# Kernel tuning notes

Hardware: AMD Instinct MI355X
Metric: run time of the kernel (lower is better)

Reference implementation:

```python
import jax, jax.numpy as jnp
import numpy as np

B, N, C = 2, 2048, 1024
H, HD = 16, 64
PX, PY, PS = 24, 24, 16  # S2RoPE head_dim split (px+py+ps == head_dim)


def rotate_half(t):
    t1, t2 = jnp.split(t, 2, axis=-1)
    return jnp.concatenate([-t2, t1], axis=-1)


def apply_phase_rope(t, phase):
    # t: [B, N, H, d_seg] (d_seg even), phase: [B, N, d_seg//2] angles in radians
    ang = jnp.concatenate([phase, phase], axis=-1)[:, :, None, :]  # [B,N,1,d_seg]
    return t * jnp.cos(ang) + rotate_half(t) * jnp.sin(ang)


def s2rope(t, phase_x, phase_y, phase_sph):
    # spherical RoPE: rotate three disjoint segments of head_dim by the
    # per-token x / y / spherical phases
    tx, ty, ts = t[..., :PX], t[..., PX:PX + PY], t[..., PX + PY:]
    return jnp.concatenate([
        apply_phase_rope(tx, phase_x),
        apply_phase_rope(ty, phase_y),
        apply_phase_rope(ts, phase_sph),
    ], axis=-1)


def setup_inputs() -> dict:
    key = jax.random.key(0)
    ks = jax.random.split(key, 9)
    two_pi = 6.2831853
    return {
        "x": jax.random.normal(ks[0], (B, N, C), dtype=jnp.float32),
        "phase_x": jax.random.uniform(ks[1], (B, N, PX // 2), dtype=jnp.float32) * two_pi,
        "phase_y": jax.random.uniform(ks[2], (B, N, PY // 2), dtype=jnp.float32) * two_pi,
        "phase_sph": jax.random.uniform(ks[3], (B, N, PS // 2), dtype=jnp.float32) * two_pi,
        "rope_mask": jax.random.randint(ks[4], (B, N), 0, 2).astype(bool),
        "Wqkv": jax.random.normal(ks[5], (C, 3 * C), dtype=jnp.float32) * (C ** -0.5),
        "bqkv": jax.random.normal(ks[6], (3 * C,), dtype=jnp.float32) * 0.02,
        "Wproj": jax.random.normal(ks[7], (C, C), dtype=jnp.float32) * (C ** -0.5),
        "bproj": jax.random.normal(ks[8], (C,), dtype=jnp.float32) * 0.02,
    }


def reference(x, phase_x, phase_y, phase_sph, rope_mask, Wqkv, bqkv, Wproj, bproj):
    # qkv projection -> [B, N, 3, H, HD]
    qkv = (x @ Wqkv + bqkv).reshape(B, N, 3, H, HD)
    q, k, v = qkv[:, :, 0], qkv[:, :, 1], qkv[:, :, 2]  # each [B, N, H, HD]

    # template path: S2RoPE with rope_mask selecting which tokens are rotated
    q_rope = s2rope(q, phase_x, phase_y, phase_sph)
    k_rope = s2rope(k, phase_x, phase_y, phase_sph)
    m = rope_mask[:, :, None, None]  # [B, N, 1, 1]
    q = jnp.where(m, q_rope, q)
    k = jnp.where(m, k_rope, k)

    scale = HD ** -0.5
    # [B, H, N, N] scores, softmax over keys, then weighted sum of values
    attn = jax.nn.softmax(jnp.einsum('bnhd,bmhd->bhnm', q, k) * scale, axis=-1)
    out = jnp.einsum('bhnm,bmhd->bnhd', attn, v).reshape(B, N, C)
    return out @ Wproj + bproj
```

## Files before the change

### kernel.cpp

```cpp
#include <hip/hip_runtime.h>
#include <hip/hip_fp16.h>

typedef _Float16 f16;
typedef unsigned int u32;
typedef _Float16 f16x4 __attribute__((ext_vector_type(4)));
typedef _Float16 f16x8 __attribute__((ext_vector_type(8)));
typedef float f32x4 __attribute__((ext_vector_type(4)));
typedef float f32x16 __attribute__((ext_vector_type(16)));

#define B_  2
#define N_  2048
#define C_  1024
#define H_  16
#define HD_ 64

__device__ __forceinline__ void gload_lds16(const void* g, void* l) {
  __builtin_amdgcn_global_load_lds((const __attribute__((address_space(1))) u32*)g,
                                   (__attribute__((address_space(3))) u32*)l,
                                   16, 0, 0);
}

__device__ __forceinline__ u32 pack_f16(float a, float b) {
  auto h2 = __builtin_amdgcn_cvt_pkrtz(a, b);
  return __builtin_bit_cast(u32, h2);
}

__device__ __forceinline__ float max3f(float a, float b, float c) {
  return fmaxf(fmaxf(a, b), c);
}

__global__ void detect_mask(const u32* __restrict__ m, int* __restrict__ flag) {
  __shared__ int bad;
  if (threadIdx.x == 0) bad = 0;
  __syncthreads();
  int v = 0;
  for (int i = threadIdx.x; i < 1024; i += 256) {
    u32 w = m[i];
    if (w != 0u && w != 1u && w != 0x3F800000u) v = 1;
  }
  if (v) atomicOr(&bad, 1);
  __syncthreads();
  if (threadIdx.x == 0) *flag = bad;
}

__global__ __launch_bounds__(256) void phase_tab(const float* __restrict__ px,
                                                 const float* __restrict__ py,
                                                 const float* __restrict__ psp,
                                                 const void* __restrict__ maskPtr,
                                                 const int* __restrict__ maskFlag,
                                                 float* __restrict__ cs_tab,
                                                 float* __restrict__ sn_tab) {
  const int idx = blockIdx.x * 256 + threadIdx.x;
  const int j = idx & 31, tn = idx >> 5;
  const int byteMode = *maskFlag;
  const bool doRope = byteMode ? (((const unsigned char*)maskPtr)[tn] != 0)
                               : (((const u32*)maskPtr)[tn] != 0u);
  float c = 1.f, s = 0.f;
  if (doRope) {
    float ph;
    if (j < 12)      ph = px[tn * 12 + j];
    else if (j < 24) ph = py[tn * 12 + (j - 12)];
    else             ph = psp[tn * 8 + (j - 24)];
    c = __cosf(ph);
    s = __sinf(ph);
  }
  cs_tab[idx] = c;
  sn_tab[idx] = s;
}

__global__ __launch_bounds__(256) void cvt_x(const float* __restrict__ in,
                                             f16* __restrict__ out, int n8) {
  const int i = blockIdx.x * 256 + threadIdx.x;
  if (i >= n8) return;
  const float4 a = ((const float4*)in)[i * 2];
  const float4 b = ((const float4*)in)[i * 2 + 1];
  f16x8 o = {(f16)a.x, (f16)a.y, (f16)a.z, (f16)a.w,
             (f16)b.x, (f16)b.y, (f16)b.z, (f16)b.w};
  ((f16x8*)out)[i] = o;
}

__global__ __launch_bounds__(256) void transpose_cvt(const float* __restrict__ W,
                                                     f16* __restrict__ Wt,
                                                     int R, int Ccols) {
  __shared__ __align__(16) f16 tile[32][34];
  const int c0 = blockIdx.x * 32, r0 = blockIdx.y * 32;
  const int tx = threadIdx.x, ty = threadIdx.y;
#pragma unroll
  for (int k = 0; k < 4; ++k)
    tile[ty + 8 * k][tx] = (f16)W[(size_t)(r0 + ty + 8 * k) * Ccols + c0 + tx];
  __syncthreads();
#pragma unroll
  for (int k = 0; k < 4; ++k)
    Wt[(size_t)(c0 + ty + 8 * k) * R + r0 + tx] = tile[tx][ty + 8 * k];
}

__global__ __launch_bounds__(256) void gemm_qkv(const f16* __restrict__ A,
                                                const f16* __restrict__ Bt,
                                                const float* __restrict__ bias,
                                                const float* __restrict__ cs_tab,
                                                const float* __restrict__ sn_tab,
                                                f16* __restrict__ Qh,
                                                f16* __restrict__ Kh,
                                                f16* __restrict__ Vt) {
  __shared__ __align__(16) f16 smem[128 * 130];
  f16* const As = smem;
  f16* const Bs = smem + 8192;
  const int K = 1024, Ncols = 3072;
  const int tid = threadIdx.x;
  const int lane = tid & 63;
  const int wv = tid >> 6;
  const int wm = wv >> 1, wn = wv & 1;
  const int nTN = Ncols >> 7;
  int bid = blockIdx.x;
  const int cpx = gridDim.x >> 3;
  bid = (bid & 7) * cpx + (bid >> 3);
  const int tM = bid / nTN, tN = bid % nTN;
  const int rowBase = tM << 7, colBase = tN << 7;
  const int cl = lane & 15, cg = lane >> 4;

  f32x4 acc[4][4];
#pragma unroll
  for (int i = 0; i < 4; ++i)
#pragma unroll
    for (int j = 0; j < 4; ++j) acc[i][j] = (f32x4){0.f, 0.f, 0.f, 0.f};

  const int sR = tid >> 3, sC = tid & 7;

  for (int k0 = 0; k0 < K; k0 += 64) {
#pragma unroll
    for (int is = 0; is < 4; ++is) {
      const int r = is * 32 + sR;
      const int sc = sC ^ (r & 7);
      gload_lds16(A + (size_t)(rowBase + r) * K + k0 + sc * 8, As + is * 2048 + tid * 8);
    }
#pragma unroll
    for (int is = 0; is < 4; ++is) {
      const int r = is * 32 + sR;
      const int sc = sC ^ (r & 7);
      gload_lds16(Bt + (size_t)(colBase + r) * K + k0 + sc * 8, Bs + is * 2048 + tid * 8);
    }
    asm volatile("s_waitcnt vmcnt(0)" ::: "memory");
    __syncthreads();

#pragma unroll
    for (int ks = 0; ks < 2; ++ks) {
      f16x8 af[4], bf[4];
#pragma unroll
      for (int m = 0; m < 4; ++m) {
        const int row = wm * 64 + m * 16 + cl;
        const int ck = (ks * 4 + cg) ^ (row & 7);
        af[m] = *(const f16x8*)(As + row * 64 + ck * 8);
      }
#pragma unroll
      for (int n = 0; n < 4; ++n) {
        const int row = wn * 64 + n * 16 + cl;
        const int ck = (ks * 4 + cg) ^ (row & 7);
        bf[n] = *(const f16x8*)(Bs + row * 64 + ck * 8);
      }
#pragma unroll
      for (int m = 0; m < 4; ++m)
#pragma unroll
        for (int n = 0; n < 4; ++n)
          acc[m][n] = __builtin_amdgcn_mfma_f32_16x16x32_f16(af[m], bf[n], acc[m][n], 0, 0, 0);
    }
    __syncthreads();
  }

#pragma unroll
  for (int m = 0; m < 4; ++m)
#pragma unroll
    for (int n = 0; n < 4; ++n) {
      const int lc = wn * 64 + n * 16 + cl;
      const float bz = bias[colBase + lc];
#pragma unroll
      for (int reg = 0; reg < 4; ++reg) {
        const int lr = wm * 64 + m * 16 + cg * 4 + reg;
        smem[lr * 130 + lc] = (f16)(acc[m][n][reg] + bz);
      }
    }
  __syncthreads();

  const int sec = colBase >> 10;
  const int h0 = (colBase & 1023) >> 6;
  const int bb = rowBase >> 11;
  const int nbase = rowBase & 2047;

  if (sec < 2) {
    const int lr = tid >> 1, hh = tid & 1;
    const int n = nbase + lr;
    const int h = h0 + hh;
    const f16* srcrow = smem + lr * 130 + hh * 64;
    float t[64];
#pragma unroll
    for (int c = 0; c < 8; ++c) {
      f16x8 v = *(const f16x8*)(srcrow + c * 8);
#pragma unroll
      for (int j = 0; j < 8; ++j) t[c * 8 + j] = (float)v[j];
    }
    const float* csr = cs_tab + ((size_t)bb * N_ + n) * 32;
    const float* snr = sn_tab + ((size_t)bb * N_ + n) * 32;
    __align__(16) f16 o[64];
#pragma unroll
    for (int d = 0; d < 64; ++d) {
      int j;
      float rot;
      if (d < 24) {
        j = (d < 12) ? d : d - 12;
        rot = (d < 12) ? -t[d + 12] : t[d - 12];
      } else if (d < 48) {
        const int dd = d - 24;
        j = 12 + ((dd < 12) ? dd : dd - 12);
        rot = (dd < 12) ? -t[d + 12] : t[d - 12];
      } else {
        const int dd = d - 48;
        j = 24 + ((dd < 8) ? dd : dd - 8);
        rot = (dd < 8) ? -t[d + 8] : t[d - 8];
      }
      o[d] = (f16)(t[d] * csr[j] + rot * snr[j]);
    }
    f16* dst = (sec == 0 ? Qh : Kh) + (((size_t)(bb * H_ + h)) * N_ + n) * 64;
#pragma unroll
    for (int c = 0; c < 8; ++c) *(f16x8*)(dst + c * 8) = *(const f16x8*)(o + c * 8);
  } else {
    const int pr = tid >> 1, half = tid & 1;
    const int hh = pr >> 6, d = pr & 63;
    const int h = h0 + hh;
    __align__(16) f16 o[64];
#pragma unroll
    for (int i = 0; i < 64; ++i) o[i] = smem[(half * 64 + i) * 130 + hh * 64 + d];
    f16* dst = Vt + (((size_t)(bb * H_ + h)) * 64 + d) * N_ + nbase + half * 64;
#pragma unroll
    for (int c = 0; c < 8; ++c) *(f16x8*)(dst + c * 8) = *(const f16x8*)(o + c * 8);
  }
}

__global__ __launch_bounds__(256) void gemm_bt_f32(const f16* __restrict__ A,
                                                   const f16* __restrict__ Bt,
                                                   const float* __restrict__ bias,
                                                   float* __restrict__ Cout,
                                                   int M, int N, int K) {
  __shared__ __align__(16) f16 As[128 * 64];
  __shared__ __align__(16) f16 Bs[128 * 64];
  const int tid = threadIdx.x;
  const int lane = tid & 63;
  const int wv = tid >> 6;
  const int wm = wv >> 1, wn = wv & 1;
  const int nTN = N >> 7;
  int bid = blockIdx.x;
  const int cpx = gridDim.x >> 3;
  bid = (bid & 7) * cpx + (bid >> 3);
  const int tM = bid / nTN, tN = bid % nTN;
  const int rowBase = tM << 7, colBase = tN << 7;
  const int cl = lane & 15, cg = lane >> 4;

  f32x4 acc[4][4];
#pragma unroll
  for (int i = 0; i < 4; ++i)
#pragma unroll
    for (int j = 0; j < 4; ++j) acc[i][j] = (f32x4){0.f, 0.f, 0.f, 0.f};

  const int sR = tid >> 3, sC = tid & 7;

  for (int k0 = 0; k0 < K; k0 += 64) {
#pragma unroll
    for (int is = 0; is < 4; ++is) {
      const int r = is * 32 + sR;
      const int sc = sC ^ (r & 7);
      gload_lds16(A + (size_t)(rowBase + r) * K + k0 + sc * 8, As + is * 2048 + tid * 8);
    }
#pragma unroll
    for (int is = 0; is < 4; ++is) {
      const int r = is * 32 + sR;
      const int sc = sC ^ (r & 7);
      gload_lds16(Bt + (size_t)(colBase + r) * K + k0 + sc * 8, Bs + is * 2048 + tid * 8);
    }
    asm volatile("s_waitcnt vmcnt(0)" ::: "memory");
    __syncthreads();

#pragma unroll
    for (int ks = 0; ks < 2; ++ks) {
      f16x8 af[4], bf[4];
#pragma unroll
      for (int m = 0; m < 4; ++m) {
        const int row = wm * 64 + m * 16 + cl;
        const int ck = (ks * 4 + cg) ^ (row & 7);
        af[m] = *(const f16x8*)(As + row * 64 + ck * 8);
      }
#pragma unroll
      for (int n = 0; n < 4; ++n) {
        const int row = wn * 64 + n * 16 + cl;
        const int ck = (ks * 4 + cg) ^ (row & 7);
        bf[n] = *(const f16x8*)(Bs + row * 64 + ck * 8);
      }
#pragma unroll
      for (int m = 0; m < 4; ++m)
#pragma unroll
        for (int n = 0; n < 4; ++n)
          acc[m][n] = __builtin_amdgcn_mfma_f32_16x16x32_f16(af[m], bf[n], acc[m][n], 0, 0, 0);
    }
    __syncthreads();
  }

#pragma unroll
  for (int m = 0; m < 4; ++m) {
#pragma unroll
    for (int n = 0; n < 4; ++n) {
      const int gr0 = rowBase + wm * 64 + m * 16 + cg * 4;
      const int gc = colBase + wn * 64 + n * 16 + cl;
      const float bz = bias[gc];
#pragma unroll
      for (int reg = 0; reg < 4; ++reg)
        Cout[(size_t)(gr0 + reg) * N + gc] = acc[m][n][reg] + bz;
    }
  }
}

__global__ __launch_bounds__(256) void attn2(const f16* __restrict__ Qh,
                                             const f16* __restrict__ Kh,
                                             const f16* __restrict__ Vt,
                                             f16* __restrict__ Y) {
  __shared__ __align__(16) f16 lds_flat[3 * 8192];
  const int tid = threadIdx.x, lane = tid & 63, w = tid >> 6;
  int bid = blockIdx.x;
  bid = (bid & 7) * 64 + (bid >> 3);
  const int bh = bid >> 4, qb = bid & 15;
  const int b = bh >> 4, h = bh & 15;
  const f16* Qb = Qh + (size_t)bh * N_ * 64;
  const f16* Kb = Kh + (size_t)bh * N_ * 64;
  const f16* Vb = Vt + (size_t)bh * 64 * N_;
  const int ql = lane & 31, hi = lane >> 5;

  f16x8 qf[4];
  {
    const int qrow = qb * 128 + w * 32 + ql;
    const f16 scl = (f16)0.125f;
#pragma unroll
    for (int ks = 0; ks < 4; ++ks) {
      f16x8 v = *(const f16x8*)(Qb + (size_t)qrow * 64 + ks * 16 + hi * 8);
#pragma unroll
      for (int j = 0; j < 8; ++j) v[j] *= scl;
      qf[ks] = v;
    }
  }

  f32x16 Of[2];
#pragma unroll
  for (int d = 0; d < 2; ++d)
#pragma unroll
    for (int r = 0; r < 16; ++r) Of[d][r] = 0.f;
  float m_run = -1e30f, l_run = 0.f;

  const int sr = tid >> 3, sc = tid & 7;
#define STAGE(t, bp)                                                                     \
  {                                                                                      \
    _Pragma("unroll") for (int i = 0; i < 2; ++i) {                                      \
      const int row = i * 32 + sr;                                                       \
      const int g = sc ^ (row & 7);                                                      \
      gload_lds16(Kb + (size_t)((t) * 64 + row) * 64 + g * 8, (bp) + i * 2048 + tid * 8);\
    }                                                                                    \
    _Pragma("unroll") for (int i = 0; i < 2; ++i) {                                      \
      const int row = i * 32 + sr;                                                       \
      const int g = sc ^ (row & 7);                                                      \
      gload_lds16(Vb + (size_t)row * N_ + (t) * 64 + g * 8,                              \
                  (bp) + 4096 + i * 2048 + tid * 8);                                     \
    }                                                                                    \
  }

#define SOFTMAX_CHUNK(sa)                                                                \
  {                                                                                      \
    float t0 = max3f(sa[0], sa[1], sa[2]);                                               \
    float t1 = max3f(sa[3], sa[4], sa[5]);                                               \
    float t2 = max3f(sa[6], sa[7], sa[8]);                                               \
    float t3 = max3f(sa[9], sa[10], sa[11]);                                             \
    float t4 = max3f(sa[12], sa[13], sa[14]);                                            \
    float pmax = max3f(max3f(t0, t1, t2), max3f(t3, t4, sa[15]), -1e30f);                \
    pmax = fmaxf(pmax, __shfl_xor(pmax, 32));                                            \
    if (__any(pmax > m_run + 8.0f)) {                                                    \
      const float mnew = fmaxf(m_run, pmax);                                             \
      const float corr = __expf(m_run - mnew);                                           \
      l_run *= corr;                                                                     \
      _Pragma("unroll") for (int d = 0; d < 2; ++d)                                      \
        _Pragma("unroll") for (int r = 0; r < 16; ++r) Of[d][r] *= corr;                 \
      m_run = mnew;                                                                      \
    }                                                                                    \
    _Pragma("unroll") for (int r = 0; r < 16; ++r) sa[r] = __expf(sa[r] - m_run);        \
    float s0 = ((sa[0] + sa[1]) + (sa[2] + sa[3])) + ((sa[4] + sa[5]) + (sa[6] + sa[7]));\
    float s1 = ((sa[8] + sa[9]) + (sa[10] + sa[11])) +                                   \
               ((sa[12] + sa[13]) + (sa[14] + sa[15]));                                  \
    l_run += s0 + s1;                                                                    \
  }

#define PV_CHUNK(sa, s)                                                                  \
  {                                                                                      \
    u32 pw[8];                                                                           \
    _Pragma("unroll") for (int tt = 0; tt < 8; ++tt)                                     \
      pw[tt] = pack_f16(sa[2 * tt], sa[2 * tt + 1]);                                     \
    _Pragma("unroll") for (int kk = 0; kk < 2; ++kk) {                                   \
      u32 a0 = pw[4 * kk], a1 = pw[4 * kk + 1];                                          \
      u32 b0 = pw[4 * kk + 2], b1 = pw[4 * kk + 3];                                      \
      asm volatile("v_permlane32_swap_b32 %0, %1" : "+v"(a0), "+v"(b0));                 \
      asm volatile("v_permlane32_swap_b32 %0, %1" : "+v"(a1), "+v"(b1));                 \
      union { u32 u[4]; f16x8 v; } pf;                                                   \
      pf.u[0] = a0; pf.u[1] = a1; pf.u[2] = b0; pf.u[3] = b1;                            \
      __builtin_amdgcn_s_setprio(1);                                                     \
      _Pragma("unroll") for (int df = 0; df < 2; ++df) {                                 \
        const int d = df * 32 + ql;                                                      \
        f16x8 vf = *(const f16x8*)(Vs + d * 64 + (((s) * 4 + kk * 2 + hi) ^ (d & 7)) * 8);\
        Of[df] = __builtin_amdgcn_mfma_f32_32x32x16_f16(vf, pf.v, Of[df], 0, 0, 0);      \
      }                                                                                  \
      __builtin_amdgcn_s_setprio(0);                                                     \
    }                                                                                    \
  }

  f16* const base = &lds_flat[0];
  STAGE(0, base);
  STAGE(1, base + 8192);
  asm volatile("s_waitcnt vmcnt(4)" ::: "memory");
  __builtin_amdgcn_s_barrier();

  f16* curp = base;
  f16* stagep = base + 16384;
  for (int t = 0; t < N_ / 64; ++t) {
    if (t < N_ / 64 - 2) STAGE(t + 2, stagep);
    const f16* Ks = curp;
    const f16* Vs = curp + 4096;

    f32x16 sa0, sa1;
#pragma unroll
    for (int r = 0; r < 16; ++r) { sa0[r] = 0.f; sa1[r] = 0.f; }
    const int krow0 = ql, krow1 = 32 + ql;
    __builtin_amdgcn_s_setprio(1);
#pragma unroll
    for (int ks = 0; ks < 4; ++ks) {
      f16x8 kf = *(const f16x8*)(Ks + krow0 * 64 + ((ks * 2 + hi) ^ (krow0 & 7)) * 8);
      sa0 = __builtin_amdgcn_mfma_f32_32x32x16_f16(kf, qf[ks], sa0, 0, 0, 0);
    }
#pragma unroll
    for (int ks = 0; ks < 4; ++ks) {
      f16x8 kf = *(const f16x8*)(Ks + krow1 * 64 + ((ks * 2 + hi) ^ (krow1 & 7)) * 8);
      sa1 = __builtin_amdgcn_mfma_f32_32x32x16_f16(kf, qf[ks], sa1, 0, 0, 0);
    }
    __builtin_amdgcn_s_setprio(0);

    SOFTMAX_CHUNK(sa0);
    PV_CHUNK(sa0, 0);
    SOFTMAX_CHUNK(sa1);
    PV_CHUNK(sa1, 1);

    if (t < N_ / 64 - 2)
      asm volatile("s_waitcnt vmcnt(4) lgkmcnt(0)" ::: "memory");
    else if (t < N_ / 64 - 1)
      asm volatile("s_waitcnt vmcnt(0) lgkmcnt(0)" ::: "memory");
    else
      asm volatile("s_waitcnt lgkmcnt(0)" ::: "memory");
    __builtin_amdgcn_s_barrier();
    curp = (curp == base + 16384) ? base : curp + 8192;
    stagep = (stagep == base + 16384) ? base : stagep + 8192;
  }

  const float l_tot = l_run + __shfl_xor(l_run, 32);
  const float inv = 1.0f / l_tot;
  f16* Ow = base + w * (32 * 72);
#pragma unroll
  for (int df = 0; df < 2; ++df)
#pragma unroll
    for (int g = 0; g < 4; ++g) {
      f16x4 ov;
#pragma unroll
      for (int e = 0; e < 4; ++e) ov[e] = (f16)(Of[df][g * 4 + e] * inv);
      *(f16x4*)(Ow + ql * 72 + df * 32 + g * 8 + hi * 4) = ov;
    }
  __syncthreads();
  const int rr = lane >> 1, half = lane & 1;
  const f16* srcp = Ow + rr * 72 + half * 32;
  const int nglob = qb * 128 + w * 32 + rr;
  f16* dst = Y + ((size_t)b * N_ + nglob) * C_ + h * 64 + half * 32;
#pragma unroll
  for (int c2 = 0; c2 < 4; ++c2)
    *(f16x8*)(dst + c2 * 8) = *(const f16x8*)(srcp + c2 * 8);
}

extern "C" void kernel_launch(void* const* d_in, const int* in_sizes, int n_in,
                              void* d_out, int out_size, void* d_ws, size_t ws_size,
                              hipStream_t stream) {
  const float* x = (const float*)d_in[0];
  const float* px = (const float*)d_in[1];
  const float* py = (const float*)d_in[2];
  const float* psp = (const float*)d_in[3];
  const void* mask = (const void*)d_in[4];
  const float* Wqkv = (const float*)d_in[5];
  const float* bqkv = (const float*)d_in[6];
  const float* Wproj = (const float*)d_in[7];
  const float* bproj = (const float*)d_in[8];
  float* out = (float*)d_out;
  char* ws = (char*)d_ws;

  f16* xh     = (f16*)(ws + 0);
  f16* Wqkvt  = (f16*)(ws + 8388608);
  f16* Wprojt = (f16*)(ws + 14680064);
  f16* Qh     = (f16*)(ws + 41943040);
  f16* Kh     = (f16*)(ws + 50331648);
  f16* Vt     = (f16*)(ws + 58720256);
  f16* Yh     = (f16*)(ws + 67108864);
  int* mflag  = (int*)(ws + 75497472);
  float* cs_tab = (float*)(ws + 16777216);
  float* sn_tab = (float*)(ws + 16777216 + 524288);

  detect_mask<<<1, 256, 0, stream>>>((const u32*)mask, mflag);
  cvt_x<<<2048, 256, 0, stream>>>(x, xh, (B_ * N_ * C_) / 8);
  phase_tab<<<512, 256, 0, stream>>>(px, py, psp, mask, mflag, cs_tab, sn_tab);
  transpose_cvt<<<dim3(96, 32), dim3(32, 8), 0, stream>>>(Wqkv, Wqkvt, C_, 3 * C_);
  transpose_cvt<<<dim3(32, 32), dim3(32, 8), 0, stream>>>(Wproj, Wprojt, C_, C_);
  gemm_qkv<<<(4096 / 128) * (3072 / 128), 256, 0, stream>>>(
      xh, Wqkvt, bqkv, cs_tab, sn_tab, Qh, Kh, Vt);
  attn2<<<512, 256, 0, stream>>>(Qh, Kh, Vt, Yh);
  gemm_bt_f32<<<(4096 / 128) * (1024 / 128), 256, 0, stream>>>(
      Yh, Wprojt, bproj, out, 4096, 1024, 1024);
}
```

Measured before the change: 153.1 us.

## Split attention over two KV halves and merge partials in a combine kernel

Splits each attention block's key/value range into two halves (flash-decoding style). This doubles the grid to 1024 blocks, so the 256 CUs of MI355X get more than two waves' worth of blocks and the tail is better balanced. Each half writes a normalized partial output plus its (max, sum) to workspace, and a new combine kernel rescales and merges the two into Y. The cost is extra global traffic for partials and statistics, one more kernel launch, and repeated Q loads.

```diff
diff --git a/kernel.cpp b/kernel.cpp
--- a/kernel.cpp
+++ b/kernel.cpp
@@ -315,19 +315,23 @@
   }
 }
 
+#define NT_ 16
 __global__ __launch_bounds__(256) void attn2(const f16* __restrict__ Qh,
                                              const f16* __restrict__ Kh,
                                              const f16* __restrict__ Vt,
-                                             f16* __restrict__ Y) {
+                                             f16* __restrict__ Op,
+                                             float2* __restrict__ Ml) {
   __shared__ __align__(16) f16 lds_flat[3 * 8192];
   const int tid = threadIdx.x, lane = tid & 63, w = tid >> 6;
   int bid = blockIdx.x;
-  bid = (bid & 7) * 64 + (bid >> 3);
-  const int bh = bid >> 4, qb = bid & 15;
+  bid = (bid & 7) * 128 + (bid >> 3);
+  const int bh = bid >> 5;
+  const int qb = (bid >> 1) & 15;
+  const int kvh = bid & 1;
   const int b = bh >> 4, h = bh & 15;
   const f16* Qb = Qh + (size_t)bh * N_ * 64;
-  const f16* Kb = Kh + (size_t)bh * N_ * 64;
-  const f16* Vb = Vt + (size_t)bh * 64 * N_;
+  const f16* Kb = Kh + (size_t)bh * N_ * 64 + (size_t)kvh * 1024 * 64;
+  const f16* Vb = Vt + (size_t)bh * 64 * N_ + (size_t)kvh * 1024;
   const int ql = lane & 31, hi = lane >> 5;
 
   f16x8 qf[4];
@@ -420,8 +424,8 @@
 
   f16* curp = base;
   f16* stagep = base + 16384;
-  for (int t = 0; t < N_ / 64; ++t) {
-    if (t < N_ / 64 - 2) STAGE(t + 2, stagep);
+  for (int t = 0; t < NT_; ++t) {
+    if (t < NT_ - 2) STAGE(t + 2, stagep);
     const f16* Ks = curp;
     const f16* Vs = curp + 4096;
 
@@ -447,9 +451,9 @@
     SOFTMAX_CHUNK(sa1);
     PV_CHUNK(sa1, 1);
 
-    if (t < N_ / 64 - 2)
+    if (t < NT_ - 2)
       asm volatile("s_waitcnt vmcnt(4) lgkmcnt(0)" ::: "memory");
-    else if (t < N_ / 64 - 1)
+    else if (t < NT_ - 1)
       asm volatile("s_waitcnt vmcnt(0) lgkmcnt(0)" ::: "memory");
     else
       asm volatile("s_waitcnt lgkmcnt(0)" ::: "memory");
@@ -460,6 +464,9 @@
 
   const float l_tot = l_run + __shfl_xor(l_run, 32);
   const float inv = 1.0f / l_tot;
+  const int part = kvh * 32 + bh;
+  if (hi == 0)
+    Ml[(size_t)part * N_ + qb * 128 + w * 32 + ql] = make_float2(m_run, l_tot);
   f16* Ow = base + w * (32 * 72);
 #pragma unroll
   for (int df = 0; df < 2; ++df)
@@ -474,10 +481,38 @@
   const int rr = lane >> 1, half = lane & 1;
   const f16* srcp = Ow + rr * 72 + half * 32;
   const int nglob = qb * 128 + w * 32 + rr;
-  f16* dst = Y + ((size_t)b * N_ + nglob) * C_ + h * 64 + half * 32;
+  f16* dst = Op + ((size_t)part * N_ + nglob) * 64 + half * 32;
 #pragma unroll
   for (int c2 = 0; c2 < 4; ++c2)
     *(f16x8*)(dst + c2 * 8) = *(const f16x8*)(srcp + c2 * 8);
+}
+
+__global__ __launch_bounds__(256) void combine(const f16* __restrict__ Op,
+                                               const float2* __restrict__ Ml,
+                                               f16* __restrict__ Y) {
+  const int gid = blockIdx.x * 256 + threadIdx.x;
+  const int r = gid >> 1, part = gid & 1;
+  const int bh = r >> 11, n = r & 2047;
+  const int b = bh >> 4, h = bh & 15;
+  const float2 ml0 = Ml[(size_t)bh * N_ + n];
+  const float2 ml1 = Ml[(size_t)(32 + bh) * N_ + n];
+  const float m = fmaxf(ml0.x, ml1.x);
+  float w0 = ml0.y * __expf(ml0.x - m);
+  float w1 = ml1.y * __expf(ml1.x - m);
+  const float inv = 1.0f / (w0 + w1);
+  w0 *= inv; w1 *= inv;
+  const f16* o0 = Op + ((size_t)bh * N_ + n) * 64 + part * 32;
+  const f16* o1 = Op + ((size_t)(32 + bh) * N_ + n) * 64 + part * 32;
+  f16* dst = Y + ((size_t)b * N_ + n) * C_ + h * 64 + part * 32;
+#pragma unroll
+  for (int c = 0; c < 4; ++c) {
+    const f16x8 a = ((const f16x8*)o0)[c];
+    const f16x8 bv = ((const f16x8*)o1)[c];
+    f16x8 o;
+#pragma unroll
+    for (int j = 0; j < 8; ++j) o[j] = (f16)((float)a[j] * w0 + (float)bv[j] * w1);
+    ((f16x8*)dst)[c] = o;
+  }
 }
 
 extern "C" void kernel_launch(void* const* d_in, const int* in_sizes, int n_in,
@@ -503,8 +538,10 @@
   f16* Vt     = (f16*)(ws + 58720256);
   f16* Yh     = (f16*)(ws + 67108864);
   int* mflag  = (int*)(ws + 75497472);
-  float* cs_tab = (float*)(ws + 16777216);
-  float* sn_tab = (float*)(ws + 16777216 + 524288);
+  float*  cs_tab = (float*)(ws + 16777216);
+  float*  sn_tab = (float*)(ws + 17301504);
+  f16*    Op     = (f16*)(ws + 17825792);
+  float2* Ml     = (float2*)(ws + 34603008);
 
   detect_mask<<<1, 256, 0, stream>>>((const u32*)mask, mflag);
   cvt_x<<<2048, 256, 0, stream>>>(x, xh, (B_ * N_ * C_) / 8);
@@ -513,7 +550,8 @@
   transpose_cvt<<<dim3(32, 32), dim3(32, 8), 0, stream>>>(Wproj, Wprojt, C_, C_);
   gemm_qkv<<<(4096 / 128) * (3072 / 128), 256, 0, stream>>>(
       xh, Wqkvt, bqkv, cs_tab, sn_tab, Qh, Kh, Vt);
-  attn2<<<512, 256, 0, stream>>>(Qh, Kh, Vt, Yh);
+  attn2<<<1024, 256, 0, stream>>>(Qh, Kh, Vt, Op, Ml);
+  combine<<<512, 256, 0, stream>>>(Op, Ml, Yh);
   gemm_bt_f32<<<(4096 / 128) * (1024 / 128), 256, 0, stream>>>(
       Yh, Wprojt, bproj, out, 4096, 1024, 1024);
 }
```

Result: slower. 160.1 us (+4.6%).

## Load K and V fragments directly from global memory instead of LDS staging

Applied to the files above, without the earlier changes.

The attention kernel drops its triple-buffered async global-to-LDS staging of K and V tiles, along with the per-iteration barriers and waitcnts. Each wave now reads its K and V MFMA fragments straight from global memory, relying on L2 and cache hits since the four waves in a block share the same K/V. This removes synchronisation and LDS traffic but gives up explicit prefetch, so load latency now sits on the critical path. The V reads are strided by row across N, which can make them poorly coalesced.

```diff
diff --git a/kernel.cpp b/kernel.cpp
--- a/kernel.cpp
+++ b/kernel.cpp
@@ -315,11 +315,11 @@
   }
 }
 
-__global__ __launch_bounds__(256) void attn2(const f16* __restrict__ Qh,
+__global__ __launch_bounds__(256) void attn3(const f16* __restrict__ Qh,
                                              const f16* __restrict__ Kh,
                                              const f16* __restrict__ Vt,
                                              f16* __restrict__ Y) {
-  __shared__ __align__(16) f16 lds_flat[3 * 8192];
+  __shared__ __align__(16) f16 Owlds[4][32 * 72];
   const int tid = threadIdx.x, lane = tid & 63, w = tid >> 6;
   int bid = blockIdx.x;
   bid = (bid & 7) * 64 + (bid >> 3);
@@ -349,22 +349,6 @@
 #pragma unroll
     for (int r = 0; r < 16; ++r) Of[d][r] = 0.f;
   float m_run = -1e30f, l_run = 0.f;
-
-  const int sr = tid >> 3, sc = tid & 7;
-#define STAGE(t, bp)                                                                     \
-  {                                                                                      \
-    _Pragma("unroll") for (int i = 0; i < 2; ++i) {                                      \
-      const int row = i * 32 + sr;                                                       \
-      const int g = sc ^ (row & 7);                                                      \
-      gload_lds16(Kb + (size_t)((t) * 64 + row) * 64 + g * 8, (bp) + i * 2048 + tid * 8);\
-    }                                                                                    \
-    _Pragma("unroll") for (int i = 0; i < 2; ++i) {                                      \
-      const int row = i * 32 + sr;                                                       \
-      const int g = sc ^ (row & 7);                                                      \
-      gload_lds16(Vb + (size_t)row * N_ + (t) * 64 + g * 8,                              \
-                  (bp) + 4096 + i * 2048 + tid * 8);                                     \
-    }                                                                                    \
-  }
 
 #define SOFTMAX_CHUNK(sa)                                                                \
   {                                                                                      \
@@ -405,62 +389,45 @@
       __builtin_amdgcn_s_setprio(1);                                                     \
       _Pragma("unroll") for (int df = 0; df < 2; ++df) {                                 \
         const int d = df * 32 + ql;                                                      \
-        f16x8 vf = *(const f16x8*)(Vs + d * 64 + (((s) * 4 + kk * 2 + hi) ^ (d & 7)) * 8);\
+        f16x8 vf = *(const f16x8*)(Vb + (size_t)d * N_ + t * 64 +                        \
+                                   ((s) * 4 + kk * 2 + hi) * 8);                         \
         Of[df] = __builtin_amdgcn_mfma_f32_32x32x16_f16(vf, pf.v, Of[df], 0, 0, 0);      \
       }                                                                                  \
       __builtin_amdgcn_s_setprio(0);                                                     \
     }                                                                                    \
   }
 
-  f16* const base = &lds_flat[0];
-  STAGE(0, base);
-  STAGE(1, base + 8192);
-  asm volatile("s_waitcnt vmcnt(4)" ::: "memory");
-  __builtin_amdgcn_s_barrier();
-
-  f16* curp = base;
-  f16* stagep = base + 16384;
+#pragma unroll 2
   for (int t = 0; t < N_ / 64; ++t) {
-    if (t < N_ / 64 - 2) STAGE(t + 2, stagep);
-    const f16* Ks = curp;
-    const f16* Vs = curp + 4096;
+    const f16* Kr0 = Kb + (size_t)(t * 64 + ql) * 64 + hi * 8;
+    const f16* Kr1 = Kb + (size_t)(t * 64 + 32 + ql) * 64 + hi * 8;
+    f16x8 k0[4], k1[4];
+#pragma unroll
+    for (int ks = 0; ks < 4; ++ks) k0[ks] = *(const f16x8*)(Kr0 + ks * 16);
+#pragma unroll
+    for (int ks = 0; ks < 4; ++ks) k1[ks] = *(const f16x8*)(Kr1 + ks * 16);
 
     f32x16 sa0, sa1;
 #pragma unroll
     for (int r = 0; r < 16; ++r) { sa0[r] = 0.f; sa1[r] = 0.f; }
-    const int krow0 = ql, krow1 = 32 + ql;
     __builtin_amdgcn_s_setprio(1);
 #pragma unroll
-    for (int ks = 0; ks < 4; ++ks) {
-      f16x8 kf = *(const f16x8*)(Ks + krow0 * 64 + ((ks * 2 + hi) ^ (krow0 & 7)) * 8);
-      sa0 = __builtin_amdgcn_mfma_f32_32x32x16_f16(kf, qf[ks], sa0, 0, 0, 0);
-    }
-#pragma unroll
-    for (int ks = 0; ks < 4; ++ks) {
-      f16x8 kf = *(const f16x8*)(Ks + krow1 * 64 + ((ks * 2 + hi) ^ (krow1 & 7)) * 8);
-      sa1 = __builtin_amdgcn_mfma_f32_32x32x16_f16(kf, qf[ks], sa1, 0, 0, 0);
-    }
+    for (int ks = 0; ks < 4; ++ks)
+      sa0 = __builtin_amdgcn_mfma_f32_32x32x16_f16(k0[ks], qf[ks], sa0, 0, 0, 0);
+#pragma unroll
+    for (int ks = 0; ks < 4; ++ks)
+      sa1 = __builtin_amdgcn_mfma_f32_32x32x16_f16(k1[ks], qf[ks], sa1, 0, 0, 0);
     __builtin_amdgcn_s_setprio(0);
 
     SOFTMAX_CHUNK(sa0);
     PV_CHUNK(sa0, 0);
     SOFTMAX_CHUNK(sa1);
     PV_CHUNK(sa1, 1);
-
-    if (t < N_ / 64 - 2)
-      asm volatile("s_waitcnt vmcnt(4) lgkmcnt(0)" ::: "memory");
-    else if (t < N_ / 64 - 1)
-      asm volatile("s_waitcnt vmcnt(0) lgkmcnt(0)" ::: "memory");
-    else
-      asm volatile("s_waitcnt lgkmcnt(0)" ::: "memory");
-    __builtin_amdgcn_s_barrier();
-    curp = (curp == base + 16384) ? base : curp + 8192;
-    stagep = (stagep == base + 16384) ? base : stagep + 8192;
   }
 
   const float l_tot = l_run + __shfl_xor(l_run, 32);
   const float inv = 1.0f / l_tot;
-  f16* Ow = base + w * (32 * 72);
+  f16* Ow = &Owlds[w][0];
 #pragma unroll
   for (int df = 0; df < 2; ++df)
 #pragma unroll
@@ -504,7 +471,7 @@
   f16* Yh     = (f16*)(ws + 67108864);
   int* mflag  = (int*)(ws + 75497472);
   float* cs_tab = (float*)(ws + 16777216);
-  float* sn_tab = (float*)(ws + 16777216 + 524288);
+  float* sn_tab = (float*)(ws + 17301504);
 
   detect_mask<<<1, 256, 0, stream>>>((const u32*)mask, mflag);
   cvt_x<<<2048, 256, 0, stream>>>(x, xh, (B_ * N_ * C_) / 8);
@@ -513,7 +480,7 @@
   transpose_cvt<<<dim3(32, 32), dim3(32, 8), 0, stream>>>(Wproj, Wprojt, C_, C_);
   gemm_qkv<<<(4096 / 128) * (3072 / 128), 256, 0, stream>>>(
       xh, Wqkvt, bqkv, cs_tab, sn_tab, Qh, Kh, Vt);
-  attn2<<<512, 256, 0, stream>>>(Qh, Kh, Vt, Yh);
+  attn3<<<512, 256, 0, stream>>>(Qh, Kh, Vt, Yh);
   gemm_bt_f32<<<(4096 / 128) * (1024 / 128), 256, 0, stream>>>(
       Yh, Wprojt, bproj, out, 4096, 1024, 1024);
 }
```

After: 211.0 us. +37.8%, slower.
